# Kernel optimization log

Measured on AMD Instinct MI355X. Metric: run time of the kernel, lower is better.

## Reference

```python
import jax, jax.numpy as jnp
import numpy as np


def _bilinear_crop(feat, grid):
    """Bilinear sampling with border clamping (BilinearSamplerBHWD semantics).

    feat: [R, C, H, W] float features (one feature map per RoI)
    grid: [R, gh, gw, 2] normalized coords in [-1, 1], channel order (y, x)
    returns: [R, C, gh, gw]
    """
    R, C, H, W = feat.shape
    # unnormalize: -1 -> 0, +1 -> H-1 / W-1
    y = (grid[..., 0] + 1.0) * (H - 1) * 0.5   # [R, gh, gw]
    x = (grid[..., 1] + 1.0) * (W - 1) * 0.5

    y0 = jnp.floor(y)
    x0 = jnp.floor(x)
    wy = y - y0  # fractional parts
    wx = x - x0

    y0i = jnp.clip(y0.astype(jnp.int32), 0, H - 1)
    y1i = jnp.clip(y0.astype(jnp.int32) + 1, 0, H - 1)
    x0i = jnp.clip(x0.astype(jnp.int32), 0, W - 1)
    x1i = jnp.clip(x0.astype(jnp.int32) + 1, 0, W - 1)

    r = jnp.arange(R)[:, None, None]  # [R,1,1] broadcast over grid
    # advanced indexing -> [R, gh, gw, C]
    v00 = feat[r, :, y0i, x0i]
    v01 = feat[r, :, y0i, x1i]
    v10 = feat[r, :, y1i, x0i]
    v11 = feat[r, :, y1i, x1i]

    wy = wy[..., None]
    wx = wx[..., None]
    out = (v00 * (1 - wy) * (1 - wx) + v01 * (1 - wy) * wx
           + v10 * wy * (1 - wx) + v11 * wy * wx)  # [R, gh, gw, C]
    return jnp.transpose(out, (0, 3, 1, 2))  # [R, C, gh, gw]


def setup_inputs() -> dict:
    key = jax.random.key(0)
    k1, k2 = jax.random.split(key)
    R, C, H, W = 128, 512, 37, 37
    GS = 14  # pool_size * 2 (crop_resize_with_max_pool=True)
    input1 = jax.random.normal(k1, (R, C, H, W), dtype=jnp.float32)
    # normalized sampling grid in [-1, 1], channel order (y, x)
    input2 = jax.random.uniform(k2, (R, GS, GS, 2), dtype=jnp.float32,
                                minval=-1.0, maxval=1.0)
    return {"input1": input1, "input2": input2}


def reference(input1, input2):
    return _bilinear_crop(input1, input2)
```

## Files before the change

kernel.cpp:

```cpp
#include <hip/hip_runtime.h>
#include <hip/hip_bf16.h>
#include <stdint.h>


#define RR 128
#define CC 512
#define HH 37
#define WW 37
#define GS 14
#define NP (GS * GS)
#define PLANE (HH * WW)
#define CPB 4
#define NBLK (RR * (CC / CPB))
#define PLANE_BYTES (CPB * PLANE * 4)
#define NCHUNK ((PLANE_BYTES + 1023) / 1024)

typedef __attribute__((address_space(1))) const void gconst_void;
typedef __attribute__((address_space(3))) void lds_void;

__global__ __launch_bounds__(256) void roicrop_kernel(
    const float* __restrict__ feat,
    const float* __restrict__ grid,
    float* __restrict__ out)
{
    __shared__ float  s_plane[CPB * PLANE];
    __shared__ float4 s_pt[NP];

    const int blk = blockIdx.x;
    const int r   = blk / (CC / CPB);
    const int cb  = blk % (CC / CPB);
    const int c0  = cb * CPB;
    const int tid  = threadIdx.x;
    const int wave = tid >> 6;
    const int lane = tid & 63;

    const char* src = (const char*)(feat + ((size_t)r * CC + c0) * PLANE);
    char* lds_base = (char*)s_plane;
    #pragma unroll
    for (int ch = wave; ch < NCHUNK; ch += 4) {
        const int off = ch * 1024 + lane * 16;
        if (off + 16 <= PLANE_BYTES) {
            __builtin_amdgcn_global_load_lds(
                (gconst_void*)(src + off),
                (lds_void*)(lds_base + ch * 1024 + lane * 16),
                16, 0, 0);
        }
    }

    if (tid < NP) {
        float2 g2 = reinterpret_cast<const float2*>(grid)[(size_t)r * NP + tid];
        float y = (g2.x + 1.0f) * 18.0f;
        float x = (g2.y + 1.0f) * 18.0f;
        float y0f = floorf(y), x0f = floorf(x);
        float wy = y - y0f, wx = x - x0f;
        int y0 = (int)y0f, x0 = (int)x0f;
        int y0i = min(max(y0,     0), HH - 1);
        int y1i = min(max(y0 + 1, 0), HH - 1);
        int x0i = min(max(x0,     0), WW - 1);
        int x1i = min(max(x0 + 1, 0), WW - 1);
        uint32_t oa = (uint32_t)(y0i * WW + x0i) | ((uint32_t)(y0i * WW + x1i) << 16);
        uint32_t ob = (uint32_t)(y1i * WW + x0i) | ((uint32_t)(y1i * WW + x1i) << 16);
        s_pt[tid] = make_float4(wy, wx, __uint_as_float(oa), __uint_as_float(ob));
    }

    __syncthreads();

    if (tid < NP) {
        const int cl = tid / 49;
        const int j  = tid - cl * 49;
        const int p0 = j * 4;
        const float* pl = s_plane + cl * PLANE;
        float4 o;
        float* op = &o.x;
        #pragma unroll
        for (int k = 0; k < 4; ++k) {
            float4 pt = s_pt[p0 + k];
            uint32_t oa = __float_as_uint(pt.z);
            uint32_t ob = __float_as_uint(pt.w);
            float v00 = pl[oa & 0xffffu];
            float v01 = pl[oa >> 16];
            float v10 = pl[ob & 0xffffu];
            float v11 = pl[ob >> 16];
            float top = v00 + (v01 - v00) * pt.y;
            float bot = v10 + (v11 - v10) * pt.y;
            op[k] = top + (bot - top) * pt.x;
        }
        float4* dst = reinterpret_cast<float4*>(out + ((size_t)r * CC + c0) * NP);
        dst[tid] = o;
    }
}

extern "C" void kernel_launch(void* const* d_in, const int* in_sizes, int n_in,
                              void* d_out, int out_size, void* d_ws, size_t ws_size,
                              hipStream_t stream) {
    const float* feat = (const float*)d_in[0];
    const float* grid = (const float*)d_in[1];
    float* out = (float*)d_out;
    roicrop_kernel<<<dim3(NBLK), dim3(256), 0, stream>>>(feat, grid, out);
}
```

Baseline: 80.78 us.

## Double-buffer channel chunks in LDS with manual vmcnt waits per block

Each block now handles 32 channels instead of 4, in 8 steps. While it computes one 4-channel chunk, the async global-to-LDS load of the chunk two steps ahead is in flight, using a two-slot buffer. The grid preprocessing is hoisted and done once per 32 channels, and full __syncthreads is replaced by explicit s_waitcnt vmcnt counts plus raw barriers. This hides load latency and cuts per-block setup. In exchange it doubles LDS per block, which lowers occupancy, launches eight times fewer blocks, and relies on hand-counted vmcnt values that also count the global stores.

After: 90.45 us. 12.0% more time.

```diff
diff --git a/kernel.cpp b/kernel.cpp
--- a/kernel.cpp
+++ b/kernel.cpp
@@ -11,48 +11,59 @@
 #define NP (GS * GS)
 #define PLANE (HH * WW)
 #define CPB 4
-#define NBLK (RR * (CC / CPB))
-#define PLANE_BYTES (CPB * PLANE * 4)
-#define NCHUNK ((PLANE_BYTES + 1023) / 1024)
+#define CHUNK_BYTES (CPB * PLANE * 4)
+#define NCHUNK 22
+#define KITER 8
+#define CGROUP (CPB * KITER)
+#define NBLK (RR * (CC / CGROUP))
 
 typedef __attribute__((address_space(1))) const void gconst_void;
 typedef __attribute__((address_space(3))) void lds_void;
+
+__device__ __forceinline__ void memfence_barrier() {
+    asm volatile("" ::: "memory");
+    __builtin_amdgcn_s_barrier();
+    __builtin_amdgcn_sched_barrier(0);
+    asm volatile("" ::: "memory");
+}
+
+__device__ __forceinline__ void stage_chunk(const char* __restrict__ src,
+                                            char* dst, int wave, int lane) {
+    for (int ch = wave; ch < NCHUNK; ch += 4) {
+        const int off = ch * 1024 + lane * 16;
+        if (off + 16 <= CHUNK_BYTES) {
+            __builtin_amdgcn_global_load_lds(
+                (gconst_void*)(src + off), (lds_void*)(dst + off), 16, 0, 0);
+        }
+    }
+}
 
 __global__ __launch_bounds__(256) void roicrop_kernel(
     const float* __restrict__ feat,
     const float* __restrict__ grid,
     float* __restrict__ out)
 {
-    __shared__ float  s_plane[CPB * PLANE];
+    __shared__ float  s_buf[2][CPB * PLANE];
     __shared__ float4 s_pt[NP];
 
     const int blk = blockIdx.x;
-    const int r   = blk / (CC / CPB);
-    const int cb  = blk % (CC / CPB);
-    const int c0  = cb * CPB;
+    const int r   = blk / (CC / CGROUP);
+    const int g   = blk % (CC / CGROUP);
+    const int c0  = g * CGROUP;
     const int tid  = threadIdx.x;
     const int wave = tid >> 6;
     const int lane = tid & 63;
 
-    const char* src = (const char*)(feat + ((size_t)r * CC + c0) * PLANE);
-    char* lds_base = (char*)s_plane;
-    #pragma unroll
-    for (int ch = wave; ch < NCHUNK; ch += 4) {
-        const int off = ch * 1024 + lane * 16;
-        if (off + 16 <= PLANE_BYTES) {
-            __builtin_amdgcn_global_load_lds(
-                (gconst_void*)(src + off),
-                (lds_void*)(lds_base + ch * 1024 + lane * 16),
-                16, 0, 0);
-        }
-    }
+    const char* src0 = (const char*)(feat + ((size_t)r * CC + c0) * PLANE);
+
+    stage_chunk(src0,               (char*)s_buf[0], wave, lane);
+    stage_chunk(src0 + CHUNK_BYTES, (char*)s_buf[1], wave, lane);
 
     if (tid < NP) {
         float2 g2 = reinterpret_cast<const float2*>(grid)[(size_t)r * NP + tid];
         float y = (g2.x + 1.0f) * 18.0f;
         float x = (g2.y + 1.0f) * 18.0f;
         float y0f = floorf(y), x0f = floorf(x);
-        float wy = y - y0f, wx = x - x0f;
         int y0 = (int)y0f, x0 = (int)x0f;
         int y0i = min(max(y0,     0), HH - 1);
         int y1i = min(max(y0 + 1, 0), HH - 1);
@@ -60,33 +71,65 @@
         int x1i = min(max(x0 + 1, 0), WW - 1);
         uint32_t oa = (uint32_t)(y0i * WW + x0i) | ((uint32_t)(y0i * WW + x1i) << 16);
         uint32_t ob = (uint32_t)(y1i * WW + x0i) | ((uint32_t)(y1i * WW + x1i) << 16);
-        s_pt[tid] = make_float4(wy, wx, __uint_as_float(oa), __uint_as_float(ob));
+        s_pt[tid] = make_float4(y - y0f, x - x0f,
+                                __uint_as_float(oa), __uint_as_float(ob));
     }
 
-    __syncthreads();
+    asm volatile("s_waitcnt lgkmcnt(0)" ::: "memory");
+    if (wave < 2) asm volatile("s_waitcnt vmcnt(6)" ::: "memory");
+    else          asm volatile("s_waitcnt vmcnt(5)" ::: "memory");
+    memfence_barrier();
 
+    int cl = 0;
+    float wy[4], wx[4];
+    int o00[4], o01[4], o10[4], o11[4];
     if (tid < NP) {
-        const int cl = tid / 49;
-        const int j  = tid - cl * 49;
-        const int p0 = j * 4;
-        const float* pl = s_plane + cl * PLANE;
-        float4 o;
-        float* op = &o.x;
+        cl = tid / 49;
+        const int j = tid - cl * 49;
         #pragma unroll
-        for (int k = 0; k < 4; ++k) {
-            float4 pt = s_pt[p0 + k];
+        for (int t = 0; t < 4; ++t) {
+            float4 pt = s_pt[j * 4 + t];
+            wy[t] = pt.x; wx[t] = pt.y;
             uint32_t oa = __float_as_uint(pt.z);
             uint32_t ob = __float_as_uint(pt.w);
-            float v00 = pl[oa & 0xffffu];
-            float v01 = pl[oa >> 16];
-            float v10 = pl[ob & 0xffffu];
-            float v11 = pl[ob >> 16];
-            float top = v00 + (v01 - v00) * pt.y;
-            float bot = v10 + (v11 - v10) * pt.y;
-            op[k] = top + (bot - top) * pt.x;
+            o00[t] = oa & 0xffffu; o01[t] = oa >> 16;
+            o10[t] = ob & 0xffffu; o11[t] = ob >> 16;
         }
-        float4* dst = reinterpret_cast<float4*>(out + ((size_t)r * CC + c0) * NP);
-        dst[tid] = o;
+    }
+
+    for (int k = 0; k < KITER; ++k) {
+        if (tid < NP) {
+            const float* pl = &s_buf[k & 1][cl * PLANE];
+            float4 o;
+            #pragma unroll
+            for (int t = 0; t < 4; ++t) {
+                float v00 = pl[o00[t]];
+                float v01 = pl[o01[t]];
+                float v10 = pl[o10[t]];
+                float v11 = pl[o11[t]];
+                float top = v00 + (v01 - v00) * wx[t];
+                float bot = v10 + (v11 - v10) * wx[t];
+                (&o.x)[t] = top + (bot - top) * wy[t];
+            }
+            float4* dst = reinterpret_cast<float4*>(
+                out + ((size_t)r * CC + c0 + 4 * k) * NP);
+            dst[tid] = o;
+        }
+        memfence_barrier();
+
+        if (k < KITER - 2)
+            stage_chunk(src0 + (size_t)(k + 2) * CHUNK_BYTES,
+                        (char*)s_buf[k & 1], wave, lane);
+
+        if (k < KITER - 1) {
+            if (k < KITER - 2) {
+                if (wave < 2) asm volatile("s_waitcnt vmcnt(7)" ::: "memory");
+                else          asm volatile("s_waitcnt vmcnt(6)" ::: "memory");
+            } else {
+                asm volatile("s_waitcnt vmcnt(1)" ::: "memory");
+            }
+            memfence_barrier();
+        }
     }
 }
 
```

## Give each wave its own channel plane and drop block-wide barrier

Applied to the files above, without the earlier changes.

Each of the four waves in a block now loads one channel's feature plane into its own padded LDS slot. Every wave recomputes all 196 sampling coordinates in registers instead of sharing a table through LDS, so the __syncthreads is replaced by a per-wave vmcnt wait. Outputs are written per point with nontemporal stores, and all 256 threads take part in the interpolation. The aim is to remove cross-wave synchronisation and LDS round trips. The cost is redundant grid loads and math in every wave, plus 16-byte async loads whose per-channel source addresses are no longer 16-byte aligned.

Result: faster. 74.47 us (-7.8%).

```diff
diff --git a/kernel.cpp b/kernel.cpp
--- a/kernel.cpp
+++ b/kernel.cpp
@@ -7,13 +7,10 @@
 #define CC 512
 #define HH 37
 #define WW 37
-#define GS 14
-#define NP (GS * GS)
-#define PLANE (HH * WW)
-#define CPB 4
-#define NBLK (RR * (CC / CPB))
-#define PLANE_BYTES (CPB * PLANE * 4)
-#define NCHUNK ((PLANE_BYTES + 1023) / 1024)
+#define NP 196
+#define PLANE 1369
+#define PLANE_PAD 1376
+#define NBLK (RR * (CC / 4))
 
 typedef __attribute__((address_space(1))) const void gconst_void;
 typedef __attribute__((address_space(3))) void lds_void;
@@ -23,70 +20,74 @@
     const float* __restrict__ grid,
     float* __restrict__ out)
 {
-    __shared__ float  s_plane[CPB * PLANE];
-    __shared__ float4 s_pt[NP];
+    __shared__ float s_plane[4][PLANE_PAD];
 
     const int blk = blockIdx.x;
-    const int r   = blk / (CC / CPB);
-    const int cb  = blk % (CC / CPB);
-    const int c0  = cb * CPB;
-    const int tid  = threadIdx.x;
-    const int wave = tid >> 6;
-    const int lane = tid & 63;
+    const int r   = blk >> 7;
+    const int cb  = blk & 127;
+    const int c   = cb * 4 + (threadIdx.x >> 6);
+    const int wave = threadIdx.x >> 6;
+    const int lane = threadIdx.x & 63;
 
-    const char* src = (const char*)(feat + ((size_t)r * CC + c0) * PLANE);
-    char* lds_base = (char*)s_plane;
+    const char* srcb = (const char*)(feat + ((size_t)r * CC + c) * PLANE);
+    char* dstb = (char*)&s_plane[wave][0];
     #pragma unroll
-    for (int ch = wave; ch < NCHUNK; ch += 4) {
-        const int off = ch * 1024 + lane * 16;
-        if (off + 16 <= PLANE_BYTES) {
-            __builtin_amdgcn_global_load_lds(
-                (gconst_void*)(src + off),
-                (lds_void*)(lds_base + ch * 1024 + lane * 16),
-                16, 0, 0);
+    for (int ch = 0; ch < 5; ++ch) {
+        __builtin_amdgcn_global_load_lds(
+            (gconst_void*)(srcb + ch * 1024 + lane * 16),
+            (lds_void*)(dstb + ch * 1024 + lane * 16), 16, 0, 0);
+    }
+    if (lane < 22) {
+        __builtin_amdgcn_global_load_lds(
+            (gconst_void*)(srcb + 5120 + lane * 16),
+            (lds_void*)(dstb + 5120 + lane * 16), 16, 0, 0);
+    }
+    if (lane == 0) {
+        __builtin_amdgcn_global_load_lds(
+            (gconst_void*)(srcb + 5472 + lane * 4),
+            (lds_void*)(dstb + 5472 + lane * 4), 4, 0, 0);
+    }
+
+    const float2* gp = reinterpret_cast<const float2*>(grid) + (size_t)r * NP;
+    float wy[4], wx[4];
+    uint32_t pa[4], pb[4];
+    #pragma unroll
+    for (int t = 0; t < 4; ++t) {
+        const int p = lane + 64 * t;
+        wy[t] = 0.f; wx[t] = 0.f; pa[t] = 0; pb[t] = 0;
+        if (p < NP) {
+            float2 g2 = gp[p];
+            float y = (g2.x + 1.0f) * 18.0f;
+            float x = (g2.y + 1.0f) * 18.0f;
+            float y0f = floorf(y), x0f = floorf(x);
+            wy[t] = y - y0f; wx[t] = x - x0f;
+            int y0 = (int)y0f, x0 = (int)x0f;
+            int y0i = min(max(y0,     0), HH - 1);
+            int y1i = min(max(y0 + 1, 0), HH - 1);
+            int x0i = min(max(x0,     0), WW - 1);
+            int x1i = min(max(x0 + 1, 0), WW - 1);
+            pa[t] = (uint32_t)(y0i * WW + x0i) | ((uint32_t)(y0i * WW + x1i) << 16);
+            pb[t] = (uint32_t)(y1i * WW + x0i) | ((uint32_t)(y1i * WW + x1i) << 16);
         }
     }
 
-    if (tid < NP) {
-        float2 g2 = reinterpret_cast<const float2*>(grid)[(size_t)r * NP + tid];
-        float y = (g2.x + 1.0f) * 18.0f;
-        float x = (g2.y + 1.0f) * 18.0f;
-        float y0f = floorf(y), x0f = floorf(x);
-        float wy = y - y0f, wx = x - x0f;
-        int y0 = (int)y0f, x0 = (int)x0f;
-        int y0i = min(max(y0,     0), HH - 1);
-        int y1i = min(max(y0 + 1, 0), HH - 1);
-        int x0i = min(max(x0,     0), WW - 1);
-        int x1i = min(max(x0 + 1, 0), WW - 1);
-        uint32_t oa = (uint32_t)(y0i * WW + x0i) | ((uint32_t)(y0i * WW + x1i) << 16);
-        uint32_t ob = (uint32_t)(y1i * WW + x0i) | ((uint32_t)(y1i * WW + x1i) << 16);
-        s_pt[tid] = make_float4(wy, wx, __uint_as_float(oa), __uint_as_float(ob));
-    }
+    asm volatile("s_waitcnt vmcnt(0)" ::: "memory");
+    __builtin_amdgcn_sched_barrier(0);
 
-    __syncthreads();
-
-    if (tid < NP) {
-        const int cl = tid / 49;
-        const int j  = tid - cl * 49;
-        const int p0 = j * 4;
-        const float* pl = s_plane + cl * PLANE;
-        float4 o;
-        float* op = &o.x;
-        #pragma unroll
-        for (int k = 0; k < 4; ++k) {
-            float4 pt = s_pt[p0 + k];
-            uint32_t oa = __float_as_uint(pt.z);
-            uint32_t ob = __float_as_uint(pt.w);
-            float v00 = pl[oa & 0xffffu];
-            float v01 = pl[oa >> 16];
-            float v10 = pl[ob & 0xffffu];
-            float v11 = pl[ob >> 16];
-            float top = v00 + (v01 - v00) * pt.y;
-            float bot = v10 + (v11 - v10) * pt.y;
-            op[k] = top + (bot - top) * pt.x;
+    const float* pl = &s_plane[wave][0];
+    float* dstp = out + ((size_t)r * CC + c) * NP;
+    #pragma unroll
+    for (int t = 0; t < 4; ++t) {
+        const int p = lane + 64 * t;
+        if (p < NP) {
+            float v00 = pl[pa[t] & 0xffffu];
+            float v01 = pl[pa[t] >> 16];
+            float v10 = pl[pb[t] & 0xffffu];
+            float v11 = pl[pb[t] >> 16];
+            float top = v00 + (v01 - v00) * wx[t];
+            float bot = v10 + (v11 - v10) * wx[t];
+            __builtin_nontemporal_store(top + (bot - top) * wy[t], dstp + p);
         }
-        float4* dst = reinterpret_cast<float4*>(out + ((size_t)r * CC + c0) * NP);
-        dst[tid] = o;
     }
 }
 
```
